# Kernel tuning notes

Measured on AMD Instinct MI355X. Metric: run time of the kernel, lower is better.

The kernel has to match this reference:

```python
import jax, jax.numpy as jnp
import numpy as np

ND, NT, B = 16384, 16384, 4096
FD, FT, C = 256, 256, 768


def _gat(x_src, x_dst, ei, Ws, Wd, a_s, a_d, b, num_dst, self_loops):
    """PyG GATConv, heads=1: per-edge attention softmax over incoming edges."""
    if self_loops:
        loops = jnp.arange(num_dst, dtype=ei.dtype)
        ei = jnp.concatenate([ei, jnp.stack([loops, loops])], axis=1)
    src, dst = ei[0], ei[1]
    hs = x_src @ Ws                                   # [Ns, C]
    hd = x_dst @ Wd                                   # [Ndst, C]
    e = jax.nn.leaky_relu((hs @ a_s)[src] + (hd @ a_d)[dst], 0.2)   # [E]
    m = jax.ops.segment_max(e, dst, num_segments=num_dst)
    p = jnp.exp(e - m[dst])
    s = jax.ops.segment_sum(p, dst, num_segments=num_dst)
    alpha = p / (s[dst] + 1e-16)
    out = jax.ops.segment_sum(hs[src] * alpha[:, None], dst, num_segments=num_dst)
    return out + b


def _l2norm(x):
    n = jnp.linalg.norm(x, axis=1, keepdims=True)
    return x / jnp.maximum(n, 1e-12)


def setup_inputs() -> dict:
    ks = iter(jax.random.split(jax.random.key(0), 64))
    def nrm(shape, fan_in=None):
        s = 1.0 if fan_in is None else (1.0 / fan_in) ** 0.5
        return jax.random.normal(next(ks), shape, jnp.float32) * s
    inp = {}
    inp["x_drug"] = nrm((ND, FD))
    inp["x_target"] = nrm((NT, FT))
    inp["cell_features"] = nrm((B, 890))
    for et, fs, fd in (("dd", FD, FD), ("dt", FD, FT), ("tt", FT, FT)):
        inp[f"W_src_{et}"] = nrm((fs, C), fs)
        inp[f"W_dst_{et}"] = nrm((fd, C), fd)
        inp[f"a_src_{et}"] = nrm((C,), C)
        inp[f"a_dst_{et}"] = nrm((C,), C)
        inp[f"b_{et}"] = jnp.zeros((C,), jnp.float32)
    for name, fi, fo in (("red1", 890, 2048), ("red2", 2048, 512), ("red3", 512, 2 * C),
                         ("r2a", 4 * C, 2048), ("r2b", 2048, 512), ("r2c", 512, C), ("cls", C, 2)):
        inp[f"{name}_w"] = nrm((fi, fo), fi)
        inp[f"{name}_b"] = jnp.zeros((fo,), jnp.float32)
    inp["drug1_id"] = jax.random.randint(next(ks), (B,), 0, ND)
    inp["drug2_id"] = jax.random.randint(next(ks), (B,), 0, ND)
    inp["ei_dd"] = jax.random.randint(next(ks), (2, 131072), 0, ND)
    inp["ei_dt"] = jnp.stack([jax.random.randint(next(ks), (262144,), 0, ND),
                              jax.random.randint(next(ks), (262144,), 0, NT)])
    inp["ei_tt"] = jax.random.randint(next(ks), (2, 262144), 0, NT)
    return inp


def reference(x_drug, x_target, cell_features,
              W_src_dd, W_dst_dd, a_src_dd, a_dst_dd, b_dd,
              W_src_dt, W_dst_dt, a_src_dt, a_dst_dt, b_dt,
              W_src_tt, W_dst_tt, a_src_tt, a_dst_tt, b_tt,
              red1_w, red1_b, red2_w, red2_b, red3_w, red3_b,
              r2a_w, r2a_b, r2b_w, r2b_b, r2c_w, r2c_b,
              cls_w, cls_b,
              drug1_id, drug2_id, ei_dd, ei_dt, ei_tt):
    # HeteroConv (aggr='sum') followed by per-type ReLU, num_layers=1
    drug = jax.nn.relu(_gat(x_drug, x_drug, ei_dd,
                            W_src_dd, W_dst_dd, a_src_dd, a_dst_dd, b_dd, ND, True))
    target = jax.nn.relu(
        _gat(x_drug, x_target, ei_dt, W_src_dt, W_dst_dt, a_src_dt, a_dst_dt, b_dt, NT, False)
        + _gat(x_target, x_target, ei_tt, W_src_tt, W_dst_tt, a_src_tt, a_dst_tt, b_tt, NT, True))
    del target  # with num_layers=1 the target embeddings never feed the output (faithful)
    d1 = drug[drug1_id]
    d2 = drug[drug2_id]
    cell = _l2norm(cell_features)
    cell = jax.nn.relu(cell @ red1_w + red1_b)
    cell = jax.nn.relu(cell @ red2_w + red2_b)
    cell = jax.nn.relu(cell @ red3_w + red3_b)          # [B, 2*C]
    hidden = _l2norm(jnp.concatenate([d1, d2, cell], axis=1))  # [B, 4*C]
    hidden = jax.nn.relu(hidden @ r2a_w + r2a_b)
    hidden = jax.nn.relu(hidden @ r2b_w + r2b_b)
    hidden = jax.nn.relu(hidden @ r2c_w + r2c_b)
    return hidden @ cls_w + cls_b                       # [B, 2]
```

## Files before the change

kernel.cpp:

```cpp
#include <hip/hip_runtime.h>
#include <cstdint>

#define ND 16384
#define BATCH 4096
#define CDIM 768
#define E_DD 131072
#define FD 256

typedef unsigned short u16;
typedef u16 u16x4 __attribute__((ext_vector_type(4)));
typedef u16 u16x8 __attribute__((ext_vector_type(8)));
typedef short s16x8 __attribute__((ext_vector_type(8)));
typedef float f32x4 __attribute__((ext_vector_type(4)));

__device__ __forceinline__ u16 f2bf(float x) {
  union { float f; uint32_t u; } v; v.f = x;
  uint32_t r = v.u + 0x7fffu + ((v.u >> 16) & 1u);
  return (u16)(r >> 16);
}
__device__ __forceinline__ float bf2f(u16 h) {
  union { float f; uint32_t u; } v; v.u = ((uint32_t)h) << 16;
  return v.f;
}
__device__ __forceinline__ uint32_t split2p(float x) {
  u16 h = f2bf(x);
  u16 l = f2bf(x - bf2f(h));
  return ((uint32_t)h << 16) | l;
}

#define GLOAD_LDS16(gp, lp)                                                   \
  __builtin_amdgcn_global_load_lds(                                           \
      (__attribute__((address_space(1))) void*)(gp),                          \
      (__attribute__((address_space(3))) void*)(lp), 16, 0, 0)

#define KP 40

template <int KS, int OUT_BF16, int RELU, int BIAS, int ASPLIT, int ALO, int BLO,
          int BKD>
__device__ __forceinline__ void gemm_core(
    int bx, int by, int bz,
    const float* __restrict__ Af,
    const u16* __restrict__ Ahi, const u16* __restrict__ Alo,
    const u16* __restrict__ Bhi, const u16* __restrict__ Blo,
    const float* __restrict__ bias,
    float* __restrict__ Cf, u16* __restrict__ Chi,
    int M, int N, int K, u16* AsB, u16* BsB) {
  constexpr int MT = 4, NT = 4;
  constexpr int BM = 128, BN = 128;
  constexpr int ASEG = BM / 64;
  constexpr int BSEG = BN / 64;
  constexpr bool DIRECT = (ASPLIT == 0 && ALO == 0 && BLO == 0);

  const int t = threadIdx.x;
  const int bm0 = bx * BM, bn0 = by * BN;
  const int wid = t >> 6, lane = t & 63;
  const int quad = lane >> 4, l16 = lane & 15;
  const int wm0 = (wid >> 1) * (MT * 16);
  const int wn0 = (wid & 1) * (NT * 16);

  const int chunk = K / KS;
  const int kbeg = (KS > 1) ? bz * chunk : 0;
  const int kend = kbeg + chunk;

  float bvv[NT];
#pragma unroll
  for (int ni = 0; ni < NT; ++ni)
    bvv[ni] = BIAS ? bias[bn0 + wn0 + ni * 16 + l16] : 0.f;

  f32x4 acc[MT][NT];
#pragma unroll
  for (int i = 0; i < MT; ++i)
#pragma unroll
    for (int j = 0; j < NT; ++j) acc[i][j] = (f32x4){0.f, 0.f, 0.f, 0.f};

  if constexpr (DIRECT) {
    constexpr int SLOTS = BKD / 8;
    constexpr int SM = SLOTS - 1;
    constexpr int NLD = (BM * BKD) / (256 * 8);
    auto stageA = [&](int buf, int kk) {
#pragma unroll
      for (int c = 0; c < NLD; ++c) {
        int s = t + 256 * c;
        int r = s / SLOTS, j = s % SLOTS;
        int jj = j ^ (r & SM);
        size_t goff = (size_t)(bm0 + r) * K + kk + jj * 8;
        int lofs = __builtin_amdgcn_readfirstlane((wid * 64 + 256 * c) * 8);
        GLOAD_LDS16(Ahi + goff, AsB + buf * (BM * BKD) + lofs);
      }
    };
    auto stageB = [&](int buf, int kk) {
#pragma unroll
      for (int c = 0; c < NLD; ++c) {
        int s = t + 256 * c;
        int r = s / SLOTS, j = s % SLOTS;
        int jj = j ^ (r & SM);
        size_t goff = (size_t)(bn0 + r) * K + kk + jj * 8;
        int lofs = __builtin_amdgcn_readfirstlane((wid * 64 + 256 * c) * 8);
        GLOAD_LDS16(Bhi + goff, BsB + buf * (BN * BKD) + lofs);
      }
    };
    const int rsw = l16 & SM;
    stageA(0, kbeg);
    stageB(0, kbeg);
    int cur = 0;
    for (int k0 = kbeg;;) {
      __syncthreads();
      int kn = k0 + BKD;
      if (kn < kend) {
        stageA(cur ^ 1, kn);
        stageB(cur ^ 1, kn);
      }
      const u16* Ab = AsB + cur * (BM * BKD);
      const u16* Bb = BsB + cur * (BN * BKD);
#pragma unroll
      for (int h = 0; h < BKD / 32; ++h) {
        s16x8 ah[MT], bh[NT];
#pragma unroll
        for (int mi = 0; mi < MT; ++mi)
          ah[mi] = *(const s16x8*)(Ab + (wm0 + mi * 16 + l16) * BKD +
                                   (((h * 4 + quad) ^ rsw) * 8));
#pragma unroll
        for (int ni = 0; ni < NT; ++ni)
          bh[ni] = *(const s16x8*)(Bb + (wn0 + ni * 16 + l16) * BKD +
                                   (((h * 4 + quad) ^ rsw) * 8));
#pragma unroll
        for (int mi = 0; mi < MT; ++mi)
#pragma unroll
          for (int ni = 0; ni < NT; ++ni)
            acc[mi][ni] = __builtin_amdgcn_mfma_f32_16x16x32_bf16(
                ah[mi], bh[ni], acc[mi][ni], 0, 0, 0);
      }
      k0 = kn;
      cur ^= 1;
      if (k0 >= kend) break;
    }
  } else {
    auto As = [&](int a, int r, int k) -> u16& { return AsB[(a * BM + r) * KP + k]; };
    auto Bs = [&](int a, int r, int k) -> u16& { return BsB[(a * BN + r) * KP + k]; };

    u16x8 pAh[ASEG], pAl[ASEG], pBh[BSEG], pBl[BSEG];

    auto loadA = [&](int c, int kk) {
      int s = t + 256 * c, row = s >> 2, kq = (s & 3) * 8;
      size_t off = (size_t)(bm0 + row) * K + kk + kq;
      if (ASPLIT) {
        f32x4 v0 = *(const f32x4*)(Af + off);
        f32x4 v1 = *(const f32x4*)(Af + off + 4);
        u16x8 h, l;
#pragma unroll
        for (int e = 0; e < 4; ++e) {
          uint32_t p = split2p(v0[e]);
          h[e] = (u16)(p >> 16); l[e] = (u16)(p & 0xffffu);
          uint32_t q = split2p(v1[e]);
          h[e + 4] = (u16)(q >> 16); l[e + 4] = (u16)(q & 0xffffu);
        }
        pAh[c] = h; pAl[c] = l;
      } else {
        pAh[c] = *(const u16x8*)(Ahi + off);
        if (ALO) pAl[c] = *(const u16x8*)(Alo + off);
      }
    };
    auto loadB = [&](int c, int kk) {
      int s = t + 256 * c, row = s >> 2, kq = (s & 3) * 8;
      size_t off = (size_t)(bn0 + row) * K + kk + kq;
      pBh[c] = *(const u16x8*)(Bhi + off);
      if (BLO) pBl[c] = *(const u16x8*)(Blo + off);
    };

#pragma unroll
    for (int c = 0; c < ASEG; ++c) loadA(c, kbeg);
#pragma unroll
    for (int c = 0; c < BSEG; ++c) loadB(c, kbeg);

    for (int k0 = kbeg;;) {
      __syncthreads();
#pragma unroll
      for (int c = 0; c < ASEG; ++c) {
        int s = t + 256 * c, row = s >> 2, kq = (s & 3) * 8;
        *(u16x8*)&As(0, row, kq) = pAh[c];
        if (ALO) *(u16x8*)&As(1, row, kq) = pAl[c];
      }
#pragma unroll
      for (int c = 0; c < BSEG; ++c) {
        int s = t + 256 * c, row = s >> 2, kq = (s & 3) * 8;
        *(u16x8*)&Bs(0, row, kq) = pBh[c];
        if (BLO) *(u16x8*)&Bs(1, row, kq) = pBl[c];
      }
      __syncthreads();

      int kn = k0 + 32;
      if (kn < kend) {
#pragma unroll
        for (int c = 0; c < ASEG; ++c) loadA(c, kn);
#pragma unroll
        for (int c = 0; c < BSEG; ++c) loadB(c, kn);
      }

      s16x8 ah[MT], al[MT], bh[NT], bl[NT];
#pragma unroll
      for (int mi = 0; mi < MT; ++mi) {
        ah[mi] = *(const s16x8*)&As(0, wm0 + mi * 16 + l16, quad * 8);
        if (ALO) al[mi] = *(const s16x8*)&As(1, wm0 + mi * 16 + l16, quad * 8);
      }
#pragma unroll
      for (int ni = 0; ni < NT; ++ni) {
        bh[ni] = *(const s16x8*)&Bs(0, wn0 + ni * 16 + l16, quad * 8);
        if (BLO) bl[ni] = *(const s16x8*)&Bs(1, wn0 + ni * 16 + l16, quad * 8);
      }
#pragma unroll
      for (int mi = 0; mi < MT; ++mi)
#pragma unroll
        for (int ni = 0; ni < NT; ++ni) {
          acc[mi][ni] = __builtin_amdgcn_mfma_f32_16x16x32_bf16(
              ah[mi], bh[ni], acc[mi][ni], 0, 0, 0);
          if (BLO)
            acc[mi][ni] = __builtin_amdgcn_mfma_f32_16x16x32_bf16(
                ah[mi], bl[ni], acc[mi][ni], 0, 0, 0);
          if (ALO)
            acc[mi][ni] = __builtin_amdgcn_mfma_f32_16x16x32_bf16(
                al[mi], bh[ni], acc[mi][ni], 0, 0, 0);
        }
      k0 = kn;
      if (k0 >= kend) break;
    }
  }

  float* Cp = (KS > 1) ? Cf + (size_t)bz * M * N : Cf;
#pragma unroll
  for (int mi = 0; mi < MT; ++mi) {
#pragma unroll
    for (int ni = 0; ni < NT; ++ni) {
      int row = bm0 + wm0 + mi * 16 + quad * 4;
      int col = bn0 + wn0 + ni * 16 + l16;
#pragma unroll
      for (int r = 0; r < 4; ++r) {
        float v = acc[mi][ni][r] + bvv[ni];
        if (RELU) v = fmaxf(v, 0.f);
        size_t o = (size_t)(row + r) * N + col;
        if (OUT_BF16) Chi[o] = f2bf(v);
        else Cp[o] = v;
      }
    }
  }
}

template <int KS, int OUT_BF16, int RELU, int BIAS, int ASPLIT, int ALO, int BLO,
          int BKD>
__global__ __launch_bounds__(256) void mfma_gemm(
    const float* __restrict__ Af,
    const u16* __restrict__ Ahi, const u16* __restrict__ Alo,
    const u16* __restrict__ Bhi, const u16* __restrict__ Blo,
    const float* __restrict__ bias,
    float* __restrict__ Cf, u16* __restrict__ Chi,
    int M, int N, int K) {
  constexpr bool DIRECT = (ASPLIT == 0 && ALO == 0 && BLO == 0);
  __shared__ __align__(16) u16 AsB[DIRECT ? 2 * 128 * BKD : (ALO ? 2 : 1) * 128 * KP];
  __shared__ __align__(16) u16 BsB[DIRECT ? 2 * 128 * BKD : (BLO ? 2 : 1) * 128 * KP];
  gemm_core<KS, OUT_BF16, RELU, BIAS, ASPLIT, ALO, BLO, BKD>(
      blockIdx.x, blockIdx.y, (KS > 1) ? (int)blockIdx.z : 0,
      Af, Ahi, Alo, Bhi, Blo, bias, Cf, Chi, M, N, K, AsB, BsB);
}

__global__ __launch_bounds__(256) void dual_gemm_red1_hs(
    const u16* __restrict__ cn, const u16* __restrict__ r1T,
    const float* __restrict__ red1_b, u16* __restrict__ c1,
    const float* __restrict__ xd, const u16* __restrict__ wsrcT,
    u16* __restrict__ hs) {
  __shared__ __align__(16) u16 SMEM[16384];
  int b = blockIdx.x;
  if (b < 512) {
    gemm_core<1, 1, 1, 1, 0, 0, 0, 32>(b & 31, b >> 5, 0, nullptr, cn, nullptr,
                                       r1T, nullptr, red1_b, nullptr, c1,
                                       BATCH, 2048, 896, SMEM, SMEM + 2 * 128 * 32);
  } else {
    int b2 = b - 512;
    gemm_core<1, 1, 0, 0, 1, 1, 0, 32>(b2 & 127, b2 >> 7, 0, xd, nullptr, nullptr,
                                       wsrcT, nullptr, nullptr, nullptr, hs,
                                       ND, CDIM, FD, SMEM, SMEM + 2 * 128 * KP);
  }
}

template <int KS>
__global__ void reduce_split_ks(const float* __restrict__ P,
                                const float* __restrict__ bias,
                                u16* __restrict__ Chi, int M, int N) {
  int i = blockIdx.x * 256 + threadIdx.x;
  int total = (M * N) >> 2;
  if (i >= total) return;
  f32x4 s = ((const f32x4*)P)[i];
#pragma unroll
  for (int z = 1; z < KS; ++z) s += ((const f32x4*)P)[(size_t)z * total + i];
  int col = (i * 4) % N;
  f32x4 bv = *(const f32x4*)(bias + col);
  u16x4 h;
#pragma unroll
  for (int e = 0; e < 4; ++e) h[e] = f2bf(fmaxf(s[e] + bv[e], 0.f));
  *(u16x4*)&Chi[i * 4] = h;
}

__global__ void reduce_cls(const float* __restrict__ P,
                           const float* __restrict__ bias,
                           const float* __restrict__ clsw,
                           const float* __restrict__ clsb,
                           float* __restrict__ out) {
  int row = blockIdx.x * 4 + (threadIdx.x >> 6);
  int lane = threadIdx.x & 63;
  const f32x4* p0 = (const f32x4*)(P + (size_t)row * CDIM);
  const f32x4* p1 = (const f32x4*)(P + (size_t)BATCH * CDIM + (size_t)row * CDIM);
  float s0 = 0.f, s1 = 0.f;
#pragma unroll
  for (int i = 0; i < 3; ++i) {
    int c4 = lane + 64 * i;
    f32x4 a = p0[c4] + p1[c4];
    f32x4 bv = *(const f32x4*)(bias + c4 * 4);
#pragma unroll
    for (int e = 0; e < 4; ++e) {
      float h = fmaxf(a[e] + bv[e], 0.f);
      int c = c4 * 4 + e;
      s0 = fmaf(h, clsw[c * 2 + 0], s0);
      s1 = fmaf(h, clsw[c * 2 + 1], s1);
    }
  }
#pragma unroll
  for (int m = 32; m; m >>= 1) {
    s0 += __shfl_xor(s0, m);
    s1 += __shfl_xor(s1, m);
  }
  if (lane == 0) {
    out[row * 2 + 0] = s0 + clsb[0];
    out[row * 2 + 1] = s1 + clsb[1];
  }
}

struct TDesc {
  const float* W;
  u16* Th;
  int K, N, Kpad, start;
};
struct TPack { TDesc d[7]; };

#define P1_T 11328
#define P1_W (P1_T + 256)
#define P1_I (P1_W + 64)
__global__ __launch_bounds__(256) void prep1(
    TPack p,
    const float* __restrict__ Wsrc, const float* __restrict__ Wdst,
    const float* __restrict__ a_s, const float* __restrict__ a_d,
    float* __restrict__ wsv, float* __restrict__ wdv,
    int* __restrict__ counts, int* __restrict__ mask, int* __restrict__ cnt,
    const float* __restrict__ cellf, u16* __restrict__ cn_hi) {
  __shared__ __align__(16) float S[1088];
  int b = blockIdx.x;
  int t = threadIdx.x;
  if (b < P1_T) {
    float (*tile)[33] = (float(*)[33])S;
    int mi = 0;
#pragma unroll
    for (int i = 1; i < 7; ++i)
      if (b >= p.d[i].start) mi = i;
    TDesc dd = p.d[mi];
    int rel = b - dd.start;
    int tilesX = dd.Kpad / 32;
    int k0 = (rel % tilesX) * 32, n0 = (rel / tilesX) * 32;
    int tx = t & 31, ty = t >> 5;
#pragma unroll
    for (int i = 0; i < 4; ++i) {
      int k = k0 + ty + 8 * i, n = n0 + tx;
      tile[ty + 8 * i][tx] = (k < dd.K && n < dd.N) ? dd.W[(size_t)k * dd.N + n] : 0.f;
    }
    __syncthreads();
#pragma unroll
    for (int i = 0; i < 4; ++i) {
      int n = n0 + ty + 8 * i, k = k0 + tx;
      if (n < dd.N) dd.Th[(size_t)n * dd.Kpad + k] = f2bf(tile[tx][ty + 8 * i]);
    }
  } else if (b < P1_W) {
    int k = b - P1_T;
    float* rs = S;
    float* rd = S + 256;
    float s = 0.f, d = 0.f;
    for (int c = t; c < CDIM; c += 256) {
      s += Wsrc[(size_t)k * CDIM + c] * a_s[c];
      d += Wdst[(size_t)k * CDIM + c] * a_d[c];
    }
    rs[t] = s; rd[t] = d;
    __syncthreads();
    for (int st = 128; st; st >>= 1) {
      if (t < st) { rs[t] += rs[t + st]; rd[t] += rd[t + st]; }
      __syncthreads();
    }
    if (t == 0) { wsv[k] = rs[0]; wdv[k] = rd[0]; }
  } else if (b < P1_I) {
    int i = (b - P1_W) * 256 + t;
    if (i < ND) { counts[i] = 1; mask[i] = 0; }
    if (i == 0) *cnt = 0;
  } else {
    int row = b - P1_I;
    float* red = S;
    const float* irow = cellf + (size_t)row * 890;
    float s = 0.f;
    for (int c = t; c < 890; c += 256) { float v = irow[c]; s += v * v; }
    red[t] = s;
    __syncthreads();
    for (int st = 128; st; st >>= 1) {
      if (t < st) red[t] += red[t + st];
      __syncthreads();
    }
    float inv = 1.f / fmaxf(sqrtf(red[0]), 1e-12f);
    for (int c = t; c < 896; c += 256) {
      float v = (c < 890) ? irow[c] * inv : 0.f;
      cn_hi[(size_t)row * 896 + c] = f2bf(v);
    }
  }
}

#define P2_E (ND * FD / 1024)
#define P2_M (P2_E + BATCH / 256)
__global__ __launch_bounds__(256) void prep2(
    const float* __restrict__ x, const float* __restrict__ wsv,
    const float* __restrict__ wdv, float* __restrict__ es, float* __restrict__ ed,
    const int* __restrict__ d1, const int* __restrict__ d2, int* __restrict__ mask,
    const int* __restrict__ dst, int* __restrict__ counts) {
  int b = blockIdx.x, t = threadIdx.x;
  if (b < P2_E) {
    int i = b * 256 + t;
    int lane = t & 63;
    int row = i >> 6;
    int c4 = lane * 4;
    f32x4 v = ((const f32x4*)x)[i];
    f32x4 ws = *(const f32x4*)(wsv + c4);
    f32x4 wd = *(const f32x4*)(wdv + c4);
    float a = v[0] * ws[0] + v[1] * ws[1] + v[2] * ws[2] + v[3] * ws[3];
    float bb = v[0] * wd[0] + v[1] * wd[1] + v[2] * wd[2] + v[3] * wd[3];
#pragma unroll
    for (int m = 32; m; m >>= 1) {
      a += __shfl_xor(a, m);
      bb += __shfl_xor(bb, m);
    }
    if (lane == 0) { es[row] = a; ed[row] = bb; }
  } else if (b < P2_M) {
    int i = (b - P2_E) * 256 + t;
    mask[d1[i]] = 1;
    mask[d2[i]] = 1;
  } else {
    int e = (b - P2_M) * 256 + t;
    atomicAdd(&counts[dst[e]], 1);
  }
}

__global__ __launch_bounds__(512) void prep3(
    const int* __restrict__ mask, int* __restrict__ cnt, int* __restrict__ list,
    const int* __restrict__ counts, int* __restrict__ offsets,
    int* __restrict__ cursor, int* __restrict__ slots) {
  __shared__ int part[512];
  int b = blockIdx.x, t = threadIdx.x;
  if (b < 32) {
    int i = b * 512 + t;
    if (mask[i]) {
      int pos = atomicAdd(cnt, 1);
      list[pos] = i;
    }
  } else {
    int base = t * 32;
    int s = 0;
    for (int i = 0; i < 32; ++i) s += counts[base + i];
    part[t] = s;
    __syncthreads();
    if (t == 0) {
      int run = 0;
      for (int i = 0; i < 512; ++i) { int tmp = part[i]; part[i] = run; run += tmp; }
      offsets[ND] = run;
    }
    __syncthreads();
    int run = part[t];
    for (int i = 0; i < 32; ++i) {
      int d = base + i;
      offsets[d] = run;
      slots[run] = d;
      cursor[d] = run + 1;
      run += counts[d];
    }
  }
}

__global__ void scatter_edges(const int* __restrict__ src, const int* __restrict__ dst,
                              int* cursor, int* slots) {
  int e = blockIdx.x * 256 + threadIdx.x;
  if (e < E_DD) {
    int pos = atomicAdd(&cursor[dst[e]], 1);
    slots[pos] = src[e];
  }
}

__global__ __launch_bounds__(256) void gat_aggregate(
    const u16* __restrict__ hs, const float* __restrict__ es,
    const float* __restrict__ ed, const int* __restrict__ offsets,
    const int* __restrict__ slots, const float* __restrict__ bias,
    const int* __restrict__ list, const int* __restrict__ cnt,
    u16* __restrict__ out) {
  int idx = blockIdx.x * 4 + (threadIdx.x >> 6);
  if (idx >= *cnt) return;
  int d = list[idx];
  int lane = threadIdx.x & 63;
  int beg = offsets[d], end = offsets[d + 1];
  float edv = ed[d];
  float mx = -1e30f;
  for (int j = beg + lane; j < end; j += 64) {
    float e = es[slots[j]] + edv;
    e = e >= 0.f ? e : 0.2f * e;
    mx = fmaxf(mx, e);
  }
#pragma unroll
  for (int m = 32; m; m >>= 1) mx = fmaxf(mx, __shfl_xor(mx, m));
  float sm = 0.f;
  for (int j = beg + lane; j < end; j += 64) {
    float e = es[slots[j]] + edv;
    e = e >= 0.f ? e : 0.2f * e;
    sm += expf(e - mx);
  }
#pragma unroll
  for (int m = 32; m; m >>= 1) sm += __shfl_xor(sm, m);
  float inv = 1.f / (sm + 1e-16f);
  int c8 = lane * 8;
  int c4 = 512 + lane * 4;
  float a8[8] = {};
  float a4[4] = {};
  for (int j = beg; j < end; ++j) {
    int srcn = slots[j];
    float e = es[srcn] + edv;
    e = e >= 0.f ? e : 0.2f * e;
    float alpha = expf(e - mx) * inv;
    const u16* hrow = hs + (size_t)srcn * CDIM;
    u16x8 r8 = *(const u16x8*)(hrow + c8);
    u16x4 r4 = *(const u16x4*)(hrow + c4);
#pragma unroll
    for (int e2 = 0; e2 < 8; ++e2) a8[e2] = fmaf(alpha, bf2f(r8[e2]), a8[e2]);
#pragma unroll
    for (int e2 = 0; e2 < 4; ++e2) a4[e2] = fmaf(alpha, bf2f(r4[e2]), a4[e2]);
  }
  u16* orow = out + (size_t)d * CDIM;
  u16x8 o8;
  u16x4 o4;
#pragma unroll
  for (int e2 = 0; e2 < 8; ++e2) o8[e2] = f2bf(fmaxf(a8[e2] + bias[c8 + e2], 0.f));
#pragma unroll
  for (int e2 = 0; e2 < 4; ++e2) o4[e2] = f2bf(fmaxf(a4[e2] + bias[c4 + e2], 0.f));
  *(u16x8*)(orow + c8) = o8;
  *(u16x4*)(orow + c4) = o4;
}

__global__ __launch_bounds__(256) void hidden_build_bf16(
    const u16* __restrict__ drug, const u16* __restrict__ c3,
    const int* __restrict__ d1, const int* __restrict__ d2,
    u16* __restrict__ hhi) {
  int row = blockIdx.x;
  int t = threadIdx.x;
  const u16* s1 = drug + (size_t)d1[row] * CDIM;
  const u16* s2 = drug + (size_t)d2[row] * CDIM;
  const u16* s3 = c3 + (size_t)row * (2 * CDIM);
  float vals[12];
  float ss = 0.f;
#pragma unroll
  for (int i = 0; i < 12; ++i) {
    int c = t + 256 * i;
    float v;
    if (i < 3)      v = bf2f(s1[c]);
    else if (i < 6) v = bf2f(s2[c - CDIM]);
    else            v = bf2f(s3[c - 2 * CDIM]);
    vals[i] = v;
    ss += v * v;
  }
  __shared__ float red[256];
  red[t] = ss;
  __syncthreads();
  for (int st = 128; st; st >>= 1) {
    if (t < st) red[t] += red[t + st];
    __syncthreads();
  }
  float inv = 1.f / fmaxf(sqrtf(red[0]), 1e-12f);
  u16* hrow_h = hhi + (size_t)row * (4 * CDIM);
#pragma unroll
  for (int i = 0; i < 12; ++i) hrow_h[t + 256 * i] = f2bf(vals[i] * inv);
}

extern "C" void kernel_launch(void* const* d_in, const int* in_sizes, int n_in,
                              void* d_out, int out_size, void* d_ws, size_t ws_size,
                              hipStream_t stream) {
  const float* x_drug   = (const float*)d_in[0];
  const float* cellf    = (const float*)d_in[2];
  const float* W_src_dd = (const float*)d_in[3];
  const float* W_dst_dd = (const float*)d_in[4];
  const float* a_src_dd = (const float*)d_in[5];
  const float* a_dst_dd = (const float*)d_in[6];
  const float* b_dd     = (const float*)d_in[7];
  const float* red1_w = (const float*)d_in[18];
  const float* red1_b = (const float*)d_in[19];
  const float* red2_w = (const float*)d_in[20];
  const float* red2_b = (const float*)d_in[21];
  const float* red3_w = (const float*)d_in[22];
  const float* red3_b = (const float*)d_in[23];
  const float* r2a_w  = (const float*)d_in[24];
  const float* r2a_b  = (const float*)d_in[25];
  const float* r2b_w  = (const float*)d_in[26];
  const float* r2b_b  = (const float*)d_in[27];
  const float* r2c_w  = (const float*)d_in[28];
  const float* r2c_b  = (const float*)d_in[29];
  const float* cls_w  = (const float*)d_in[30];
  const float* cls_b  = (const float*)d_in[31];
  const int* drug1_id = (const int*)d_in[32];
  const int* drug2_id = (const int*)d_in[33];
  const int* ei_dd    = (const int*)d_in[34];
  float* out = (float*)d_out;

  const int* dd_src = ei_dd;
  const int* dd_dst = ei_dd + E_DD;

  char* w = (char*)d_ws;
  size_t off = 0;
  auto alloc = [&](size_t bytes) -> char* {
    char* p = w + off;
    off = (off + bytes + 255) & ~(size_t)255;
    return p;
  };
  u16* hs   = (u16*)alloc((size_t)ND * CDIM * 2);
  u16* drug = (u16*)alloc((size_t)ND * CDIM * 2);
  u16* c3   = (u16*)alloc((size_t)BATCH * 2 * CDIM * 2);
  float* P  = (float*)alloc((size_t)4 * BATCH * 512 * 4);
  u16* hid_hi = hs;
  u16* cn_hi = (u16*)alloc((size_t)BATCH * 896 * 2);
  u16* c1_hi = (u16*)alloc((size_t)BATCH * 2048 * 2);
  u16* c2_hi = (u16*)alloc((size_t)BATCH * 512 * 2);
  u16* wsrcT_hi = (u16*)alloc((size_t)CDIM * FD * 2);
  u16* r1T_hi = (u16*)alloc((size_t)2048 * 896 * 2);
  u16* r2T_hi = (u16*)alloc((size_t)512 * 2048 * 2);
  u16* r3T_hi = (u16*)alloc((size_t)1536 * 512 * 2);
  u16* raT_hi = (u16*)alloc((size_t)2048 * 3072 * 2);
  u16* rbT_hi = (u16*)alloc((size_t)512 * 2048 * 2);
  u16* rcT_hi = (u16*)alloc((size_t)768 * 512 * 2);
  float* es  = (float*)alloc((size_t)ND * 4);
  float* ed  = (float*)alloc((size_t)ND * 4);
  float* wsv = (float*)alloc(FD * 4);
  float* wdv = (float*)alloc(FD * 4);
  int* counts  = (int*)alloc((size_t)ND * 4);
  int* offsets = (int*)alloc((size_t)(ND + 1) * 4);
  int* cursor  = (int*)alloc((size_t)ND * 4);
  int* slots   = (int*)alloc((size_t)(E_DD + ND) * 4);
  int* mask    = (int*)alloc((size_t)ND * 4);
  int* list    = (int*)alloc((size_t)ND * 4);
  int* cnt     = (int*)alloc(256);
  (void)ws_size; (void)n_in; (void)in_sizes; (void)out_size;

  TPack tp;
  tp.d[0] = {W_src_dd, wsrcT_hi, 256, 768, 256, 0};
  tp.d[1] = {red1_w, r1T_hi, 890, 2048, 896, 192};
  tp.d[2] = {red2_w, r2T_hi, 2048, 512, 2048, 1984};
  tp.d[3] = {red3_w, r3T_hi, 512, 1536, 512, 3008};
  tp.d[4] = {r2a_w, raT_hi, 3072, 2048, 3072, 3776};
  tp.d[5] = {r2b_w, rbT_hi, 2048, 512, 2048, 9920};
  tp.d[6] = {r2c_w, rcT_hi, 512, 768, 512, 10944};
  prep1<<<15744, 256, 0, stream>>>(tp, W_src_dd, W_dst_dd, a_src_dd, a_dst_dd,
                                   wsv, wdv, counts, mask, cnt, cellf, cn_hi);

  prep2<<<4624, 256, 0, stream>>>(x_drug, wsv, wdv, es, ed, drug1_id, drug2_id,
                                  mask, dd_dst, counts);

  prep3<<<33, 512, 0, stream>>>(mask, cnt, list, counts, offsets, cursor, slots);
  scatter_edges<<<E_DD / 256, 256, 0, stream>>>(dd_src, dd_dst, cursor, slots);

  dual_gemm_red1_hs<<<1280, 256, 0, stream>>>(cn_hi, r1T_hi, red1_b, c1_hi,
                                              x_drug, wsrcT_hi, hs);

  mfma_gemm<4, 0, 0, 0, 0, 0, 0, 64><<<dim3(BATCH / 128, 512 / 128, 4), 256, 0, stream>>>(
      nullptr, c1_hi, nullptr, r2T_hi, nullptr, nullptr, P, nullptr, BATCH, 512, 2048);
  reduce_split_ks<4><<<BATCH * 512 / 1024, 256, 0, stream>>>(P, red2_b, c2_hi, BATCH, 512);
  mfma_gemm<1, 1, 1, 1, 0, 0, 0, 64><<<dim3(BATCH / 128, 1536 / 128), 256, 0, stream>>>(
      nullptr, c2_hi, nullptr, r3T_hi, nullptr, red3_b, nullptr, c3, BATCH, 1536, 512);

  gat_aggregate<<<ND / 4, 256, 0, stream>>>(hs, es, ed, offsets, slots, b_dd, list, cnt, drug);

  hidden_build_bf16<<<BATCH, 256, 0, stream>>>(drug, c3, drug1_id, drug2_id, hid_hi);

  mfma_gemm<1, 1, 1, 1, 0, 0, 0, 64><<<dim3(BATCH / 128, 2048 / 128), 256, 0, stream>>>(
      nullptr, hid_hi, nullptr, raT_hi, nullptr, r2a_b, nullptr, c1_hi, BATCH, 2048, 3072);
  mfma_gemm<4, 0, 0, 0, 0, 0, 0, 64><<<dim3(BATCH / 128, 512 / 128, 4), 256, 0, stream>>>(
      nullptr, c1_hi, nullptr, rbT_hi, nullptr, nullptr, P, nullptr, BATCH, 512, 2048);
  reduce_split_ks<4><<<BATCH * 512 / 1024, 256, 0, stream>>>(P, r2b_b, c2_hi, BATCH, 512);
  mfma_gemm<2, 0, 0, 0, 0, 0, 0, 64><<<dim3(BATCH / 128, CDIM / 128, 2), 256, 0, stream>>>(
      nullptr, c2_hi, nullptr, rcT_hi, nullptr, nullptr, P, nullptr, BATCH, CDIM, 512);
  reduce_cls<<<BATCH / 4, 256, 0, stream>>>(P, r2c_b, cls_w, cls_b, out);
}
```

Before: 442.9 us.

## Fuse edge scatter into red1/hs GEMM launch and GAT aggregation into red2 GEMM

New measurement: 445.0 us. Within noise of the previous version (+0.5%).

```diff
diff --git a/kernel.cpp b/kernel.cpp
--- a/kernel.cpp
+++ b/kernel.cpp
@@ -261,22 +261,108 @@
       Af, Ahi, Alo, Bhi, Blo, bias, Cf, Chi, M, N, K, AsB, BsB);
 }
 
-__global__ __launch_bounds__(256) void dual_gemm_red1_hs(
+__device__ __forceinline__ void gat_body(
+    int idx, int t,
+    const u16* __restrict__ hs, const float* __restrict__ es,
+    const float* __restrict__ ed, const int* __restrict__ offsets,
+    const int* __restrict__ slots, const float* __restrict__ bias,
+    const int* __restrict__ list, const int* __restrict__ cnt,
+    u16* __restrict__ out) {
+  if (idx >= *cnt) return;
+  int d = list[idx];
+  int lane = t & 63;
+  int beg = offsets[d], end = offsets[d + 1];
+  float edv = ed[d];
+  float mx = -1e30f;
+  for (int j = beg + lane; j < end; j += 64) {
+    float e = es[slots[j]] + edv;
+    e = e >= 0.f ? e : 0.2f * e;
+    mx = fmaxf(mx, e);
+  }
+#pragma unroll
+  for (int m = 32; m; m >>= 1) mx = fmaxf(mx, __shfl_xor(mx, m));
+  float sm = 0.f;
+  for (int j = beg + lane; j < end; j += 64) {
+    float e = es[slots[j]] + edv;
+    e = e >= 0.f ? e : 0.2f * e;
+    sm += expf(e - mx);
+  }
+#pragma unroll
+  for (int m = 32; m; m >>= 1) sm += __shfl_xor(sm, m);
+  float inv = 1.f / (sm + 1e-16f);
+  int c8 = lane * 8;
+  int c4 = 512 + lane * 4;
+  float a8[8] = {};
+  float a4[4] = {};
+  for (int j = beg; j < end; ++j) {
+    int srcn = slots[j];
+    float e = es[srcn] + edv;
+    e = e >= 0.f ? e : 0.2f * e;
+    float alpha = expf(e - mx) * inv;
+    const u16* hrow = hs + (size_t)srcn * CDIM;
+    u16x8 r8 = *(const u16x8*)(hrow + c8);
+    u16x4 r4 = *(const u16x4*)(hrow + c4);
+#pragma unroll
+    for (int e2 = 0; e2 < 8; ++e2) a8[e2] = fmaf(alpha, bf2f(r8[e2]), a8[e2]);
+#pragma unroll
+    for (int e2 = 0; e2 < 4; ++e2) a4[e2] = fmaf(alpha, bf2f(r4[e2]), a4[e2]);
+  }
+  u16* orow = out + (size_t)d * CDIM;
+  u16x8 o8;
+  u16x4 o4;
+#pragma unroll
+  for (int e2 = 0; e2 < 8; ++e2) o8[e2] = f2bf(fmaxf(a8[e2] + bias[c8 + e2], 0.f));
+#pragma unroll
+  for (int e2 = 0; e2 < 4; ++e2) o4[e2] = f2bf(fmaxf(a4[e2] + bias[c4 + e2], 0.f));
+  *(u16x8*)(orow + c8) = o8;
+  *(u16x4*)(orow + c4) = o4;
+}
+
+__global__ __launch_bounds__(256) void dual_gemm_red1_hs_scatter(
     const u16* __restrict__ cn, const u16* __restrict__ r1T,
     const float* __restrict__ red1_b, u16* __restrict__ c1,
     const float* __restrict__ xd, const u16* __restrict__ wsrcT,
-    u16* __restrict__ hs) {
+    u16* __restrict__ hs,
+    const int* __restrict__ src, const int* __restrict__ dst,
+    int* __restrict__ cursor, int* __restrict__ slots) {
   __shared__ __align__(16) u16 SMEM[16384];
   int b = blockIdx.x;
   if (b < 512) {
     gemm_core<1, 1, 1, 1, 0, 0, 0, 32>(b & 31, b >> 5, 0, nullptr, cn, nullptr,
                                        r1T, nullptr, red1_b, nullptr, c1,
                                        BATCH, 2048, 896, SMEM, SMEM + 2 * 128 * 32);
-  } else {
+  } else if (b < 1280) {
     int b2 = b - 512;
     gemm_core<1, 1, 0, 0, 1, 1, 0, 32>(b2 & 127, b2 >> 7, 0, xd, nullptr, nullptr,
                                        wsrcT, nullptr, nullptr, nullptr, hs,
                                        ND, CDIM, FD, SMEM, SMEM + 2 * 128 * KP);
+  } else {
+    int e = (b - 1280) * 256 + threadIdx.x;
+    if (e < E_DD) {
+      int pos = atomicAdd(&cursor[dst[e]], 1);
+      slots[pos] = src[e];
+    }
+  }
+}
+
+__global__ __launch_bounds__(256) void red2_gat(
+    const u16* __restrict__ c1, const u16* __restrict__ r2T,
+    float* __restrict__ P,
+    const u16* __restrict__ hs, const float* __restrict__ es,
+    const float* __restrict__ ed, const int* __restrict__ offsets,
+    const int* __restrict__ slots, const float* __restrict__ bias,
+    const int* __restrict__ list, const int* __restrict__ cnt,
+    u16* __restrict__ drug) {
+  __shared__ __align__(16) u16 SMEM[16384];
+  int b = blockIdx.x;
+  if (b < 512) {
+    gemm_core<4, 0, 0, 0, 0, 0, 0, 32>(b & 31, (b >> 5) & 3, b >> 7,
+                                       nullptr, c1, nullptr, r2T, nullptr,
+                                       nullptr, P, nullptr,
+                                       BATCH, 512, 2048, SMEM, SMEM + 2 * 128 * 32);
+  } else {
+    gat_body((b - 512) * 4 + (threadIdx.x >> 6), threadIdx.x,
+             hs, es, ed, offsets, slots, bias, list, cnt, drug);
   }
 }
 
@@ -481,72 +567,6 @@
       run += counts[d];
     }
   }
-}
-
-__global__ void scatter_edges(const int* __restrict__ src, const int* __restrict__ dst,
-                              int* cursor, int* slots) {
-  int e = blockIdx.x * 256 + threadIdx.x;
-  if (e < E_DD) {
-    int pos = atomicAdd(&cursor[dst[e]], 1);
-    slots[pos] = src[e];
-  }
-}
-
-__global__ __launch_bounds__(256) void gat_aggregate(
-    const u16* __restrict__ hs, const float* __restrict__ es,
-    const float* __restrict__ ed, const int* __restrict__ offsets,
-    const int* __restrict__ slots, const float* __restrict__ bias,
-    const int* __restrict__ list, const int* __restrict__ cnt,
-    u16* __restrict__ out) {
-  int idx = blockIdx.x * 4 + (threadIdx.x >> 6);
-  if (idx >= *cnt) return;
-  int d = list[idx];
-  int lane = threadIdx.x & 63;
-  int beg = offsets[d], end = offsets[d + 1];
-  float edv = ed[d];
-  float mx = -1e30f;
-  for (int j = beg + lane; j < end; j += 64) {
-    float e = es[slots[j]] + edv;
-    e = e >= 0.f ? e : 0.2f * e;
-    mx = fmaxf(mx, e);
-  }
-#pragma unroll
-  for (int m = 32; m; m >>= 1) mx = fmaxf(mx, __shfl_xor(mx, m));
-  float sm = 0.f;
-  for (int j = beg + lane; j < end; j += 64) {
-    float e = es[slots[j]] + edv;
-    e = e >= 0.f ? e : 0.2f * e;
-    sm += expf(e - mx);
-  }
-#pragma unroll
-  for (int m = 32; m; m >>= 1) sm += __shfl_xor(sm, m);
-  float inv = 1.f / (sm + 1e-16f);
-  int c8 = lane * 8;
-  int c4 = 512 + lane * 4;
-  float a8[8] = {};
-  float a4[4] = {};
-  for (int j = beg; j < end; ++j) {
-    int srcn = slots[j];
-    float e = es[srcn] + edv;
-    e = e >= 0.f ? e : 0.2f * e;
-    float alpha = expf(e - mx) * inv;
-    const u16* hrow = hs + (size_t)srcn * CDIM;
-    u16x8 r8 = *(const u16x8*)(hrow + c8);
-    u16x4 r4 = *(const u16x4*)(hrow + c4);
-#pragma unroll
-    for (int e2 = 0; e2 < 8; ++e2) a8[e2] = fmaf(alpha, bf2f(r8[e2]), a8[e2]);
-#pragma unroll
-    for (int e2 = 0; e2 < 4; ++e2) a4[e2] = fmaf(alpha, bf2f(r4[e2]), a4[e2]);
-  }
-  u16* orow = out + (size_t)d * CDIM;
-  u16x8 o8;
-  u16x4 o4;
-#pragma unroll
-  for (int e2 = 0; e2 < 8; ++e2) o8[e2] = f2bf(fmaxf(a8[e2] + bias[c8 + e2], 0.f));
-#pragma unroll
-  for (int e2 = 0; e2 < 4; ++e2) o4[e2] = f2bf(fmaxf(a4[e2] + bias[c4 + e2], 0.f));
-  *(u16x8*)(orow + c8) = o8;
-  *(u16x4*)(orow + c4) = o4;
 }
 
 __global__ __launch_bounds__(256) void hidden_build_bf16(
@@ -665,18 +685,17 @@
                                   mask, dd_dst, counts);
 
   prep3<<<33, 512, 0, stream>>>(mask, cnt, list, counts, offsets, cursor, slots);
-  scatter_edges<<<E_DD / 256, 256, 0, stream>>>(dd_src, dd_dst, cursor, slots);
-
-  dual_gemm_red1_hs<<<1280, 256, 0, stream>>>(cn_hi, r1T_hi, red1_b, c1_hi,
-                                              x_drug, wsrcT_hi, hs);
-
-  mfma_gemm<4, 0, 0, 0, 0, 0, 0, 64><<<dim3(BATCH / 128, 512 / 128, 4), 256, 0, stream>>>(
-      nullptr, c1_hi, nullptr, r2T_hi, nullptr, nullptr, P, nullptr, BATCH, 512, 2048);
+
+  dual_gemm_red1_hs_scatter<<<1792, 256, 0, stream>>>(
+      cn_hi, r1T_hi, red1_b, c1_hi, x_drug, wsrcT_hi, hs,
+      dd_src, dd_dst, cursor, slots);
+
+  red2_gat<<<4608, 256, 0, stream>>>(c1_hi, r2T_hi, P,
+                                     hs, es, ed, offsets, slots, b_dd, list,
+                                     cnt, drug);
   reduce_split_ks<4><<<BATCH * 512 / 1024, 256, 0, stream>>>(P, red2_b, c2_hi, BATCH, 512);
   mfma_gemm<1, 1, 1, 1, 0, 0, 0, 64><<<dim3(BATCH / 128, 1536 / 128), 256, 0, stream>>>(
       nullptr, c2_hi, nullptr, r3T_hi, nullptr, red3_b, nullptr, c3, BATCH, 1536, 512);
-
-  gat_aggregate<<<ND / 4, 256, 0, stream>>>(hs, es, ed, offsets, slots, b_dd, list, cnt, drug);
 
   hidden_build_bf16<<<BATCH, 256, 0, stream>>>(drug, c3, drug1_id, drug2_id, hid_hi);
 
```
